# Optimization experiments

Measured on AMD Instinct MI355X. Metric: run time of the kernel, lower is better.

The kernel has to match this reference:

```python
import jax, jax.numpy as jnp
import numpy as np

EPS = 1e-12  # F.normalize eps


def setup_inputs() -> dict:
    key = jax.random.key(0)
    k1, k2, k3 = jax.random.split(key, 3)
    N, C, H, W, K = 64, 512, 28, 28, 64
    x = jax.random.normal(k1, (N, C, H, W), dtype=jnp.float32)
    conv_w = jax.random.normal(k2, (K, C), dtype=jnp.float32)  # 1x1 conv weight squeezed
    centroids = jax.random.uniform(k3, (K, C), dtype=jnp.float32)  # torch.rand init
    return {"x": x, "conv_w": conv_w, "centroids": centroids}


def reference(x, conv_w, centroids):
    N, C, H, W = x.shape
    K = centroids.shape[0]
    xf = x.reshape(N, C, H * W)                                  # (N, C, L)
    # 1x1 conv == matmul over channels, softmax over cluster dim
    logits = jnp.einsum('kc,ncl->nkl', conv_w, xf)               # (N, K, L)
    a = jax.nn.softmax(logits, axis=1)                           # softmax over clusters
    # vlad[n,k,c] = sum_l a[n,k,l] * (x[n,c,l] - cent[k,c])
    #            = (a @ x^T)[n,k,c] - (sum_l a[n,k,l]) * cent[k,c]
    agg = jnp.einsum('nkl,ncl->nkc', a, xf)                      # (N, K, C)
    vlad = agg - a.sum(axis=-1)[..., None] * centroids[None]     # (N, K, C)
    # intra-normalize per cluster (dim=2)
    vlad = vlad / jnp.maximum(jnp.linalg.norm(vlad, axis=2, keepdims=True), EPS)
    v = vlad.reshape(N, K * C)
    # global L2 normalize
    v = v / jnp.maximum(jnp.linalg.norm(v, axis=1, keepdims=True), EPS)
    return v
```

## Files before the change

kernel.cpp:

```cpp
#include <hip/hip_runtime.h>

#define C_ 512
#define L_ 784
#define K_ 64
#define EPS_ 1e-12f

typedef _Float16 half_t;
typedef _Float16 half8 __attribute__((ext_vector_type(8)));
typedef _Float16 half4 __attribute__((ext_vector_type(4)));
typedef float float4v __attribute__((ext_vector_type(4)));

__global__ __launch_bounds__(256) void kA(const float* __restrict__ x,
                                          const float* __restrict__ w,
                                          half_t* __restrict__ a_out,
                                          float* __restrict__ asum_part) {
    __shared__ half_t wh[64 * 72];
    __shared__ half_t xh[16 * 72];
    __shared__ float  sl[64 * 17];
    const int t    = threadIdx.x;
    const int n    = blockIdx.y;
    const int lt   = blockIdx.x;
    const int l0   = lt * 16;
    const int wv   = t >> 6;
    const int lane = t & 63;
    const int m16  = lane & 15;
    const int q    = lane >> 4;

    float4v acc = {0.f, 0.f, 0.f, 0.f};

    const float* xb = x + (size_t)n * (C_ * L_) + l0;

    for (int cc = 0; cc < 8; ++cc) {
        const int c0 = cc * 64;
#pragma unroll
        for (int i = 0; i < 4; i++) {
            int e = t + 256 * i;
            int k = e >> 4;
            int cq = e & 15;
            float4v f = *(const float4v*)(w + (size_t)k * C_ + c0 + 4 * cq);
            half4 h = { (half_t)f.x, (half_t)f.y, (half_t)f.z, (half_t)f.w };
            *(half4*)&wh[k * 72 + 4 * cq] = h;
        }
        {
            int c  = t >> 2;
            int lq = t & 3;
            float4v f = *(const float4v*)(xb + (size_t)(c0 + c) * L_ + 4 * lq);
            xh[(4 * lq + 0) * 72 + c] = (half_t)f.x;
            xh[(4 * lq + 1) * 72 + c] = (half_t)f.y;
            xh[(4 * lq + 2) * 72 + c] = (half_t)f.z;
            xh[(4 * lq + 3) * 72 + c] = (half_t)f.w;
        }
        __syncthreads();
#pragma unroll
        for (int s = 0; s < 2; s++) {
            half8 A = *(const half8*)&wh[(wv * 16 + m16) * 72 + 32 * s + 8 * q];
            half8 B = *(const half8*)&xh[m16 * 72 + 32 * s + 8 * q];
            acc = __builtin_amdgcn_mfma_f32_16x16x32_f16(A, B, acc, 0, 0, 0);
        }
        __syncthreads();
    }

#pragma unroll
    for (int r = 0; r < 4; r++)
        sl[(wv * 16 + q * 4 + r) * 17 + m16] = acc[r];
    __syncthreads();

    if (t < 16) {
        const int l = t;
        float mx = -1e30f;
        for (int k = 0; k < 64; k++) mx = fmaxf(mx, sl[k * 17 + l]);
        float s = 0.f;
        for (int k = 0; k < 64; k++) {
            float e = __expf(sl[k * 17 + l] - mx);
            sl[k * 17 + l] = e;
            s += e;
        }
        float inv = 1.f / s;
        for (int k = 0; k < 64; k++) sl[k * 17 + l] *= inv;
    }
    __syncthreads();

    if (t < 64) {
        float s = 0.f;
        for (int l = 0; l < 16; l++) s += sl[t * 17 + l];
        asum_part[((size_t)n * 49 + lt) * 64 + t] = s;
    }

    {
        int k = t >> 2, lq = t & 3;
        half4 h = { (half_t)sl[k * 17 + 4 * lq],     (half_t)sl[k * 17 + 4 * lq + 1],
                    (half_t)sl[k * 17 + 4 * lq + 2], (half_t)sl[k * 17 + 4 * lq + 3] };
        *(half4*)(a_out + (size_t)n * (K_ * L_) + (size_t)k * L_ + l0 + 4 * lq) = h;
    }
}

__global__ __launch_bounds__(256) void kB(const float* __restrict__ x,
                                          const half_t* __restrict__ a_in,
                                          float* __restrict__ agg) {
    __shared__ half_t ah[64 * 40];
    __shared__ half_t xh[64 * 40];
    const int t    = threadIdx.x;
    const int n    = blockIdx.y;
    const int c0   = blockIdx.x * 64;
    const int wv   = t >> 6;
    const int lane = t & 63;
    const int m16  = lane & 15;
    const int q    = lane >> 4;

    float4v acc[4] = {{0.f,0.f,0.f,0.f},{0.f,0.f,0.f,0.f},{0.f,0.f,0.f,0.f},{0.f,0.f,0.f,0.f}};

    const float*  xb = x   + (size_t)n * (C_ * L_);
    const half_t* ab = a_in + (size_t)n * (K_ * L_);

    for (int ltile = 0; ltile < 25; ++ltile) {
        const int l0 = ltile * 32;
        {
            int k = t >> 2, lq8 = t & 3;
            int l = l0 + 8 * lq8;
            half8 h;
            if (l < L_) h = *(const half8*)(ab + (size_t)k * L_ + l);
            else        h = (half8)(half_t)0.f;
            *(half8*)&ah[k * 40 + 8 * lq8] = h;
        }
#pragma unroll
        for (int i = 0; i < 2; i++) {
            int e = t + 256 * i;
            int c = e >> 3, lq = e & 7;
            int l = l0 + 4 * lq;
            half4 h;
            if (l < L_) {
                float4v f = *(const float4v*)(xb + (size_t)(c0 + c) * L_ + l);
                h = half4{ (half_t)f.x, (half_t)f.y, (half_t)f.z, (half_t)f.w };
            } else {
                h = half4{ (half_t)0.f, (half_t)0.f, (half_t)0.f, (half_t)0.f };
            }
            *(half4*)&xh[c * 40 + 4 * lq] = h;
        }
        __syncthreads();
        {
            half8 A = *(const half8*)&ah[(wv * 16 + m16) * 40 + 8 * q];
#pragma unroll
            for (int ct = 0; ct < 4; ct++) {
                half8 B = *(const half8*)&xh[(ct * 16 + m16) * 40 + 8 * q];
                acc[ct] = __builtin_amdgcn_mfma_f32_16x16x32_f16(A, B, acc[ct], 0, 0, 0);
            }
        }
        __syncthreads();
    }

    float* ap = agg + (size_t)n * (K_ * C_);
#pragma unroll
    for (int ct = 0; ct < 4; ct++)
#pragma unroll
        for (int r = 0; r < 4; r++)
            ap[(size_t)(wv * 16 + q * 4 + r) * C_ + c0 + ct * 16 + m16] = acc[ct][r];
}

__global__ __launch_bounds__(256) void kC(const float* __restrict__ agg,
                                          const float* __restrict__ cent,
                                          const float* __restrict__ asum_part,
                                          float* __restrict__ out) {
    __shared__ float asumS[8];
    const int t  = threadIdx.x;
    const int n  = blockIdx.y;
    const int k0 = blockIdx.x * 8;
    if (t < 8) {
        float s = 0.f;
        for (int j = 0; j < 49; j++) s += asum_part[((size_t)n * 49 + j) * 64 + k0 + t];
        asumS[t] = s;
    }
    __syncthreads();
    const int wv = t >> 6;
    const int lane = t & 63;
    for (int r = wv; r < 8; r += 4) {
        const int k = k0 + r;
        const float as = asumS[r];
        const float* ap = agg + (size_t)n * (K_ * C_) + (size_t)k * C_;
        const float* cp = cent + (size_t)k * C_;
        float v[8];
        float ss = 0.f;
#pragma unroll
        for (int j = 0; j < 8; j++) {
            int c = lane + 64 * j;
            float val = ap[c] - as * cp[c];
            v[j] = val;
            ss += val * val;
        }
#pragma unroll
        for (int off = 32; off; off >>= 1) ss += __shfl_xor(ss, off, 64);
        float scale = 1.f / (fmaxf(sqrtf(ss), EPS_) * 8.f);
        float* op = out + (size_t)n * (K_ * C_) + (size_t)k * C_;
#pragma unroll
        for (int j = 0; j < 8; j++) op[lane + 64 * j] = v[j] * scale;
    }
}

extern "C" void kernel_launch(void* const* d_in, const int* in_sizes, int n_in,
                              void* d_out, int out_size, void* d_ws, size_t ws_size,
                              hipStream_t stream) {
    (void)in_sizes; (void)n_in; (void)out_size; (void)ws_size;
    const float* x    = (const float*)d_in[0];
    const float* w    = (const float*)d_in[1];
    const float* cent = (const float*)d_in[2];
    float* out = (float*)d_out;

    char* base = (char*)d_ws;
    half_t* a    = (half_t*)base;
    float*  agg  = (float*)(base + ((size_t)K_ * L_ * 64 * 2 + 255) / 256 * 256);
    float*  asum = agg + (size_t)64 * K_ * C_;

    kA<<<dim3(49, 64), 256, 0, stream>>>(x, w, a, asum);
    kB<<<dim3(8, 64),  256, 0, stream>>>(x, a, agg);
    kC<<<dim3(8, 64),  256, 0, stream>>>(agg, cent, asum, out);
}
```

Before: 208.6 us.

## Enlarge L tiles, keep weights in registers, prefetch x loads in both GEMM kernels

```diff
diff --git a/kernel.cpp b/kernel.cpp
--- a/kernel.cpp
+++ b/kernel.cpp
@@ -14,91 +14,127 @@
                                           const float* __restrict__ w,
                                           half_t* __restrict__ a_out,
                                           float* __restrict__ asum_part) {
-    __shared__ half_t wh[64 * 72];
-    __shared__ half_t xh[16 * 72];
-    __shared__ float  sl[64 * 17];
+    __shared__ union {
+        half_t xh[64 * 72];
+        float  sl[64 * 65];
+    } sm;
     const int t    = threadIdx.x;
     const int n    = blockIdx.y;
     const int lt   = blockIdx.x;
-    const int l0   = lt * 16;
+    const int l0   = lt * 64;
+    const int lw   = (L_ - l0 < 64) ? (L_ - l0) : 64;
     const int wv   = t >> 6;
     const int lane = t & 63;
     const int m16  = lane & 15;
     const int q    = lane >> 4;
 
-    float4v acc = {0.f, 0.f, 0.f, 0.f};
+    half8 wf[16];
+    {
+        const float* wr = w + (size_t)(16 * wv + m16) * C_ + 8 * q;
+#pragma unroll
+        for (int cc = 0; cc < 16; cc++) {
+            float4v f0 = *(const float4v*)(wr + 32 * cc);
+            float4v f1 = *(const float4v*)(wr + 32 * cc + 4);
+            wf[cc] = half8{(half_t)f0.x, (half_t)f0.y, (half_t)f0.z, (half_t)f0.w,
+                           (half_t)f1.x, (half_t)f1.y, (half_t)f1.z, (half_t)f1.w};
+        }
+    }
+
+    float4v acc[4] = {{0.f,0.f,0.f,0.f},{0.f,0.f,0.f,0.f},{0.f,0.f,0.f,0.f},{0.f,0.f,0.f,0.f}};
 
     const float* xb = x + (size_t)n * (C_ * L_) + l0;
+    const int sc = t >> 4, slq = t & 15;
+
+    float4v fx[4];
+#pragma unroll
+    for (int i = 0; i < 4; i++) {
+        int c = sc, lq = slq;
+        c = sc + 16 * i;
+        float4v f = {0.f, 0.f, 0.f, 0.f};
+        if (4 * lq < lw) f = *(const float4v*)(xb + (size_t)c * L_ + 4 * lq);
+        fx[i] = f;
+    }
 
     for (int cc = 0; cc < 8; ++cc) {
-        const int c0 = cc * 64;
 #pragma unroll
         for (int i = 0; i < 4; i++) {
-            int e = t + 256 * i;
-            int k = e >> 4;
-            int cq = e & 15;
-            float4v f = *(const float4v*)(w + (size_t)k * C_ + c0 + 4 * cq);
-            half4 h = { (half_t)f.x, (half_t)f.y, (half_t)f.z, (half_t)f.w };
-            *(half4*)&wh[k * 72 + 4 * cq] = h;
-        }
-        {
-            int c  = t >> 2;
-            int lq = t & 3;
-            float4v f = *(const float4v*)(xb + (size_t)(c0 + c) * L_ + 4 * lq);
-            xh[(4 * lq + 0) * 72 + c] = (half_t)f.x;
-            xh[(4 * lq + 1) * 72 + c] = (half_t)f.y;
-            xh[(4 * lq + 2) * 72 + c] = (half_t)f.z;
-            xh[(4 * lq + 3) * 72 + c] = (half_t)f.w;
-        }
-        __syncthreads();
+            int c = sc + 16 * i;
+            int l = 4 * slq;
+            sm.xh[(l + 0) * 72 + c] = (half_t)fx[i].x;
+            sm.xh[(l + 1) * 72 + c] = (half_t)fx[i].y;
+            sm.xh[(l + 2) * 72 + c] = (half_t)fx[i].z;
+            sm.xh[(l + 3) * 72 + c] = (half_t)fx[i].w;
+        }
+        __syncthreads();
+        if (cc < 7) {
+            const float* xc = xb + (size_t)(cc + 1) * 64 * L_;
+#pragma unroll
+            for (int i = 0; i < 4; i++) {
+                int c = sc + 16 * i;
+                float4v f = {0.f, 0.f, 0.f, 0.f};
+                if (4 * slq < lw) f = *(const float4v*)(xc + (size_t)c * L_ + 4 * slq);
+                fx[i] = f;
+            }
+        }
 #pragma unroll
         for (int s = 0; s < 2; s++) {
-            half8 A = *(const half8*)&wh[(wv * 16 + m16) * 72 + 32 * s + 8 * q];
-            half8 B = *(const half8*)&xh[m16 * 72 + 32 * s + 8 * q];
-            acc = __builtin_amdgcn_mfma_f32_16x16x32_f16(A, B, acc, 0, 0, 0);
-        }
-        __syncthreads();
-    }
-
-#pragma unroll
-    for (int r = 0; r < 4; r++)
-        sl[(wv * 16 + q * 4 + r) * 17 + m16] = acc[r];
+            half8 A = wf[2 * cc + s];
+#pragma unroll
+            for (int jt = 0; jt < 4; jt++) {
+                half8 B = *(const half8*)&sm.xh[(16 * jt + m16) * 72 + 32 * s + 8 * q];
+                acc[jt] = __builtin_amdgcn_mfma_f32_16x16x32_f16(A, B, acc[jt], 0, 0, 0);
+            }
+        }
+        __syncthreads();
+    }
+
+#pragma unroll
+    for (int jt = 0; jt < 4; jt++)
+#pragma unroll
+        for (int r = 0; r < 4; r++)
+            sm.sl[(16 * wv + 4 * q + r) * 65 + 16 * jt + m16] = acc[jt][r];
     __syncthreads();
 
-    if (t < 16) {
+    if (t < 64 && t < lw) {
         const int l = t;
         float mx = -1e30f;
-        for (int k = 0; k < 64; k++) mx = fmaxf(mx, sl[k * 17 + l]);
+        for (int k = 0; k < 64; k++) mx = fmaxf(mx, sm.sl[k * 65 + l]);
         float s = 0.f;
         for (int k = 0; k < 64; k++) {
-            float e = __expf(sl[k * 17 + l] - mx);
-            sl[k * 17 + l] = e;
+            float e = __expf(sm.sl[k * 65 + l] - mx);
+            sm.sl[k * 65 + l] = e;
             s += e;
         }
         float inv = 1.f / s;
-        for (int k = 0; k < 64; k++) sl[k * 17 + l] *= inv;
+        for (int k = 0; k < 64; k++) sm.sl[k * 65 + l] *= inv;
     }
     __syncthreads();
 
     if (t < 64) {
         float s = 0.f;
-        for (int l = 0; l < 16; l++) s += sl[t * 17 + l];
-        asum_part[((size_t)n * 49 + lt) * 64 + t] = s;
-    }
-
-    {
-        int k = t >> 2, lq = t & 3;
-        half4 h = { (half_t)sl[k * 17 + 4 * lq],     (half_t)sl[k * 17 + 4 * lq + 1],
-                    (half_t)sl[k * 17 + 4 * lq + 2], (half_t)sl[k * 17 + 4 * lq + 3] };
-        *(half4*)(a_out + (size_t)n * (K_ * L_) + (size_t)k * L_ + l0 + 4 * lq) = h;
-    }
-}
-
-__global__ __launch_bounds__(256) void kB(const float* __restrict__ x,
+        for (int l = 0; l < lw; l++) s += sm.sl[t * 65 + l];
+        asum_part[((size_t)n * 13 + lt) * 64 + t] = s;
+    }
+
+    half_t* ao = a_out + (size_t)n * (K_ * L_);
+#pragma unroll
+    for (int i = 0; i < 4; i++) {
+        int u = t + 256 * i;
+        int k = u >> 4, lq = u & 15;
+        int l = 4 * lq;
+        if (l < lw) {
+            half4 h = { (half_t)sm.sl[k * 65 + l],     (half_t)sm.sl[k * 65 + l + 1],
+                        (half_t)sm.sl[k * 65 + l + 2], (half_t)sm.sl[k * 65 + l + 3] };
+            *(half4*)(ao + (size_t)k * L_ + l0 + l) = h;
+        }
+    }
+}
+
+__global__ __launch_bounds__(512) void kB(const float* __restrict__ x,
                                           const half_t* __restrict__ a_in,
                                           float* __restrict__ agg) {
-    __shared__ half_t ah[64 * 40];
-    __shared__ half_t xh[64 * 40];
+    __shared__ half_t ah[64 * 72];
+    __shared__ half_t xh[64 * 72];
     const int t    = threadIdx.x;
     const int n    = blockIdx.y;
     const int c0   = blockIdx.x * 64;
@@ -106,54 +142,73 @@
     const int lane = t & 63;
     const int m16  = lane & 15;
     const int q    = lane >> 4;
-
-    float4v acc[4] = {{0.f,0.f,0.f,0.f},{0.f,0.f,0.f,0.f},{0.f,0.f,0.f,0.f},{0.f,0.f,0.f,0.f}};
-
-    const float*  xb = x   + (size_t)n * (C_ * L_);
+    const int kw   = wv & 3;
+    const int ch   = wv >> 2;
+
+    float4v acc[2] = {{0.f,0.f,0.f,0.f},{0.f,0.f,0.f,0.f}};
+
+    const float*  xb = x    + (size_t)n * (C_ * L_);
     const half_t* ab = a_in + (size_t)n * (K_ * L_);
 
-    for (int ltile = 0; ltile < 25; ++ltile) {
-        const int l0 = ltile * 32;
-        {
-            int k = t >> 2, lq8 = t & 3;
-            int l = l0 + 8 * lq8;
-            half8 h;
-            if (l < L_) h = *(const half8*)(ab + (size_t)k * L_ + l);
-            else        h = (half8)(half_t)0.f;
-            *(half8*)&ah[k * 40 + 8 * lq8] = h;
-        }
+    const int ak = t >> 3, aho = t & 7;
+    const int xc0i = t >> 4, xlq = t & 15;
+
+    half8  pa;
+    float4v px[2];
+    {
+        int l = 8 * aho;
+        pa = (half8)(half_t)0.f;
+        if (l < L_) pa = *(const half8*)(ab + (size_t)ak * L_ + l);
 #pragma unroll
         for (int i = 0; i < 2; i++) {
-            int e = t + 256 * i;
-            int c = e >> 3, lq = e & 7;
-            int l = l0 + 4 * lq;
-            half4 h;
-            if (l < L_) {
-                float4v f = *(const float4v*)(xb + (size_t)(c0 + c) * L_ + l);
-                h = half4{ (half_t)f.x, (half_t)f.y, (half_t)f.z, (half_t)f.w };
-            } else {
-                h = half4{ (half_t)0.f, (half_t)0.f, (half_t)0.f, (half_t)0.f };
-            }
-            *(half4*)&xh[c * 40 + 4 * lq] = h;
-        }
-        __syncthreads();
-        {
-            half8 A = *(const half8*)&ah[(wv * 16 + m16) * 40 + 8 * q];
-#pragma unroll
-            for (int ct = 0; ct < 4; ct++) {
-                half8 B = *(const half8*)&xh[(ct * 16 + m16) * 40 + 8 * q];
+            int c = xc0i + 32 * i;
+            float4v f = {0.f,0.f,0.f,0.f};
+            if (4 * xlq < L_) f = *(const float4v*)(xb + (size_t)(c0 + c) * L_ + 4 * xlq);
+            px[i] = f;
+        }
+    }
+
+    for (int lt = 0; lt < 13; ++lt) {
+        *(half8*)&ah[ak * 72 + 8 * aho] = pa;
+#pragma unroll
+        for (int i = 0; i < 2; i++) {
+            int c = xc0i + 32 * i;
+            half4 h = { (half_t)px[i].x, (half_t)px[i].y, (half_t)px[i].z, (half_t)px[i].w };
+            *(half4*)&xh[c * 72 + 4 * xlq] = h;
+        }
+        __syncthreads();
+        if (lt < 12) {
+            const int l0n = (lt + 1) * 64;
+            int la = l0n + 8 * aho;
+            pa = (half8)(half_t)0.f;
+            if (la < L_) pa = *(const half8*)(ab + (size_t)ak * L_ + la);
+#pragma unroll
+            for (int i = 0; i < 2; i++) {
+                int c = xc0i + 32 * i;
+                int lx = l0n + 4 * xlq;
+                float4v f = {0.f,0.f,0.f,0.f};
+                if (lx < L_) f = *(const float4v*)(xb + (size_t)(c0 + c) * L_ + lx);
+                px[i] = f;
+            }
+        }
+#pragma unroll
+        for (int s = 0; s < 2; s++) {
+            half8 A = *(const half8*)&ah[(16 * kw + m16) * 72 + 32 * s + 8 * q];
+#pragma unroll
+            for (int ct = 0; ct < 2; ct++) {
+                half8 B = *(const half8*)&xh[(32 * ch + 16 * ct + m16) * 72 + 32 * s + 8 * q];
                 acc[ct] = __builtin_amdgcn_mfma_f32_16x16x32_f16(A, B, acc[ct], 0, 0, 0);
             }
         }
         __syncthreads();
     }
 
-    float* ap = agg + (size_t)n * (K_ * C_);
-#pragma unroll
-    for (int ct = 0; ct < 4; ct++)
+    float* ap = agg + (size_t)n * (K_ * C_) + c0;
+#pragma unroll
+    for (int ct = 0; ct < 2; ct++)
 #pragma unroll
         for (int r = 0; r < 4; r++)
-            ap[(size_t)(wv * 16 + q * 4 + r) * C_ + c0 + ct * 16 + m16] = acc[ct][r];
+            ap[(size_t)(16 * kw + 4 * q + r) * C_ + 32 * ch + 16 * ct + m16] = acc[ct][r];
 }
 
 __global__ __launch_bounds__(256) void kC(const float* __restrict__ agg,
@@ -166,7 +221,7 @@
     const int k0 = blockIdx.x * 8;
     if (t < 8) {
         float s = 0.f;
-        for (int j = 0; j < 49; j++) s += asum_part[((size_t)n * 49 + j) * 64 + k0 + t];
+        for (int j = 0; j < 13; j++) s += asum_part[((size_t)n * 13 + j) * 64 + k0 + t];
         asumS[t] = s;
     }
     __syncthreads();
@@ -209,7 +264,7 @@
     float*  agg  = (float*)(base + ((size_t)K_ * L_ * 64 * 2 + 255) / 256 * 256);
     float*  asum = agg + (size_t)64 * K_ * C_;
 
-    kA<<<dim3(49, 64), 256, 0, stream>>>(x, w, a, asum);
-    kB<<<dim3(8, 64),  256, 0, stream>>>(x, a, agg);
+    kA<<<dim3(13, 64), 256, 0, stream>>>(x, w, a, asum);
+    kB<<<dim3(8, 64),  512, 0, stream>>>(x, a, agg);
     kC<<<dim3(8, 64),  256, 0, stream>>>(agg, cent, asum, out);
 }
```

Result: no change. 211.9 us (+1.6%).
